# Performance work log

Hardware: AMD Instinct MI355X
Metric: run time of the kernel (lower is better)

## Reference

```python
import jax, jax.numpy as jnp
import numpy as np

B, N, M, K = 4, 8192, 2048, 8
F1, F2 = 256, 256


def _knn_idx(p1t, p2t, k):
    # p1t [B,N,3], p2t [B,M,3] -> idx [B,N,k] of k nearest points in p2t for each p1t point
    d = (jnp.sum(p1t ** 2, -1)[:, :, None]
         + jnp.sum(p2t ** 2, -1)[:, None, :]
         - 2.0 * jnp.einsum('bnc,bmc->bnm', p1t, p2t))
    _, idx = jax.lax.top_k(-d, k)
    return idx


def _gather(feat, idx):
    # feat [B,C,M], idx [B,N,K] -> [B,C,N,K]  (grouping_operation)
    return jax.vmap(lambda f, i: f[:, i])(feat, idx)


def setup_inputs() -> dict:
    key = jax.random.key(0)
    ks = jax.random.split(key, 16)
    rn = lambda k, s: jax.random.normal(k, s, dtype=jnp.float32)
    ru = lambda k, s: jax.random.uniform(k, s, dtype=jnp.float32)
    return {
        'pos1': rn(ks[0], (B, 3, N)),
        'pos2': rn(ks[1], (B, 3, M)),
        'feature1': rn(ks[2], (B, F1, N)),
        'feature2': rn(ks[3], (B, F2, M)),
        'w1_0': rn(ks[4], (128, F2 + 3)) * 0.05, 's1_0': ru(ks[5], (128,)), 'b1_0': rn(ks[6], (128,)) * 0.05,
        'w1_1': rn(ks[7], (128, 128)) * 0.05, 's1_1': ru(ks[8], (128,)), 'b1_1': rn(ks[9], (128,)) * 0.05,
        'w1_2': rn(ks[10], (256, 128)) * 0.05, 's1_2': ru(ks[11], (256,)), 'b1_2': rn(ks[12], (256,)) * 0.05,
        'w2_0': rn(ks[13], (256, 256 + F1)) * 0.05, 's2_0': ru(ks[14], (256,)), 'b2_0': rn(ks[15], (256,)) * 0.05,
    }


def reference(pos1, pos2, feature1, feature2,
              w1_0, s1_0, b1_0, w1_1, s1_1, b1_1, w1_2, s1_2, b1_2,
              w2_0, s2_0, b2_0):
    # KNN grouping (knn=True branch): neighbors of each pos1 point among pos2 points
    idx = _knn_idx(pos1.transpose(0, 2, 1), pos2.transpose(0, 2, 1), K)  # [B,N,K]
    pos2_grouped = _gather(pos2, idx)                 # [B,3,N,K]
    pos_diff = pos2_grouped - pos1[:, :, :, None]     # [B,3,N,K]
    feat2_grouped = _gather(feature2, idx)            # [B,F2,N,K]
    feat = jnp.concatenate([feat2_grouped, pos_diff], axis=1)  # [B,F2+3,N,K]
    # mlp1: 1x1 Conv2d (no bias) + BN(eval, folded scale/bias) + ReLU
    for w, s, b in ((w1_0, s1_0, b1_0), (w1_1, s1_1, b1_1), (w1_2, s1_2, b1_2)):
        feat = jax.nn.relu(jnp.einsum('oc,bcnk->bonk', w, feat)
                           * s[None, :, None, None] + b[None, :, None, None])
    feat = jnp.max(feat, axis=-1)                     # [B,256,N]
    feat = jnp.concatenate([feat, feature1], axis=1)  # [B,256+F1,N]
    # mlp2: 1x1 Conv1d (no bias) + BN + ReLU
    for w, s, b in ((w2_0, s2_0, b2_0),):
        feat = jax.nn.relu(jnp.einsum('oc,bcn->bon', w, feat)
                           * s[None, :, None] + b[None, :, None])
    return feat
```

## Files before the change

### kernel.cpp

```cpp
#include <hip/hip_runtime.h>
#include <hip/hip_bf16.h>

#define B_ 4
#define N_ 8192
#define M_ 2048
#define K_ 8

typedef __bf16 bf16x8 __attribute__((ext_vector_type(8)));
typedef __bf16 bf16x4 __attribute__((ext_vector_type(4)));
typedef float  floatx4 __attribute__((ext_vector_type(4)));
typedef unsigned long long u64k;

#define AS1G __attribute__((address_space(1)))
#define AS3L __attribute__((address_space(3)))

__device__ __forceinline__ void ce(u64k& a, u64k& b) {
  u64k lo = a < b ? a : b;
  u64k hi = a < b ? b : a;
  a = lo; b = hi;
}

__global__ __launch_bounds__(256) void pre_knn(
    const float* __restrict__ w10, const float* __restrict__ w11,
    const float* __restrict__ w12, const float* __restrict__ w20,
    const float* __restrict__ feature1, const float* __restrict__ feature2,
    const float* __restrict__ pos1, const float* __restrict__ pos2,
    __bf16* __restrict__ w0p, __bf16* __restrict__ w11b,
    __bf16* __restrict__ w12b, __bf16* __restrict__ w20b,
    __bf16* __restrict__ f2t, __bf16* __restrict__ f1t,
    u64k* __restrict__ part)
{
  __shared__ __align__(16) char smem[32768];
  const int bid = blockIdx.x;
  const int tid = threadIdx.x;

  if (bid < 1024) {
    floatx4* P = (floatx4*)smem;
    u64k (*md)[32] = (u64k(*)[32])(smem + 16384);
    const int b = (bid >> 7) & 3;
    const int half = bid >> 9;
    const int n0 = (bid & 127) * 64;
    const int cbase = half * 1024;

    const float* p2 = pos2 + b * 3 * M_;
    for (int i = tid; i < 1024; i += 256) {
      const int c = cbase + i;
      float x = p2[c], y = p2[M_ + c], z = p2[2 * M_ + c];
      floatx4 q;
      q[0] = x; q[1] = y; q[2] = z;
      q[3] = __fadd_rn(__fadd_rn(__fmul_rn(x, x), __fmul_rn(y, y)), __fmul_rn(z, z));
      P[i] = q;
    }
    __syncthreads();

    const int p = tid >> 2, t = tid & 3;
    const int n = n0 + p;
    const float* p1 = pos1 + b * 3 * N_;
    const float x1 = p1[n], y1 = p1[N_ + n], z1 = p1[2 * N_ + n];
    const float r1 = __fadd_rn(__fadd_rn(__fmul_rn(x1, x1), __fmul_rn(y1, y1)),
                               __fmul_rn(z1, z1));

    u64k bd[8];
    #pragma unroll
    for (int r = 0; r < 8; r++) bd[r] = ~0ULL;

    for (int bb = 0; bb < 32; ++bb) {
      floatx4 q[8];
      #pragma unroll
      for (int i = 0; i < 8; i++) q[i] = P[4 * (8 * bb + i) + t];

      u64k s[8];
      #pragma unroll
      for (int i = 0; i < 8; i++) {
        float dot = __fadd_rn(__fadd_rn(__fmul_rn(x1, q[i][0]), __fmul_rn(y1, q[i][1])),
                              __fmul_rn(z1, q[i][2]));
        float d = __fsub_rn(__fadd_rn(r1, q[i][3]), __fmul_rn(2.0f, dot));
        unsigned du = __float_as_uint(d);
        unsigned k32 = du ^ ((unsigned)((int)du >> 31) | 0x80000000u);
        s[i] = ((u64k)k32 << 11) | (unsigned)(cbase + 4 * (8 * bb + i) + t);
      }

      ce(s[0], s[1]); ce(s[2], s[3]); ce(s[4], s[5]); ce(s[6], s[7]);
      ce(s[0], s[2]); ce(s[1], s[3]); ce(s[4], s[6]); ce(s[5], s[7]);
      ce(s[1], s[2]); ce(s[5], s[6]);
      ce(s[0], s[4]); ce(s[1], s[5]); ce(s[2], s[6]); ce(s[3], s[7]);
      ce(s[2], s[4]); ce(s[3], s[5]);
      ce(s[1], s[2]); ce(s[3], s[4]); ce(s[5], s[6]);

      if (s[0] < bd[7]) {
        #pragma unroll
        for (int k = 0; k < 8; k++) { u64k x = s[7 - k]; bd[k] = bd[k] < x ? bd[k] : x; }
        ce(bd[0], bd[4]); ce(bd[1], bd[5]); ce(bd[2], bd[6]); ce(bd[3], bd[7]);
        ce(bd[0], bd[2]); ce(bd[1], bd[3]); ce(bd[4], bd[6]); ce(bd[5], bd[7]);
        ce(bd[0], bd[1]); ce(bd[2], bd[3]); ce(bd[4], bd[5]); ce(bd[6], bd[7]);
      }
    }

    {
      const int swp = (p & 3) << 3;
      #pragma unroll
      for (int r = 0; r < 8; r++) md[p][(t * 8 + r) ^ swp] = bd[r];
    }
    __syncthreads();

    if (tid < 64) {
      const int sw = tid & 3;
      const int b0 = (0 ^ sw) << 3, b1 = (1 ^ sw) << 3;
      const int b2 = (2 ^ sw) << 3, b3 = (3 ^ sw) << 3;
      int h0 = 0, h1 = 0, h2 = 0, h3 = 0;
      u64k* o = part + ((size_t)((b * 2 + half) * N_ + n0 + tid)) * 8;
      #pragma unroll
      for (int r = 0; r < 8; r++) {
        u64k k0 = md[tid][b0 + h0], k1 = md[tid][b1 + h1];
        u64k k2 = md[tid][b2 + h2], k3 = md[tid][b3 + h3];
        u64k m01 = k0 < k1 ? k0 : k1;
        u64k m23 = k2 < k3 ? k2 : k3;
        u64k m = m01 < m23 ? m01 : m23;
        h0 += (k0 == m); h1 += (k1 == m); h2 += (k2 == m); h3 += (k3 == m);
        o[r] = m;
      }
    }
  } else if (bid < 3072) {
    float (*tile)[33] = (float(*)[33])smem;
    const int tb = bid - 1024;
    const int C = 256, L = M_;
    const int b = tb >> 9;
    const int c0 = ((tb >> 6) & 7) * 32, l0 = (tb & 63) * 32;
    const int tx = tid & 31, ty = tid >> 5;
    const float* src = feature2 + (size_t)b * C * L;
    #pragma unroll
    for (int i = 0; i < 4; i++)
      tile[ty + 8 * i][tx] = src[(size_t)(c0 + ty + 8 * i) * L + l0 + tx];
    __syncthreads();
    __bf16* dst = f2t + (size_t)b * L * C;
    #pragma unroll
    for (int i = 0; i < 4; i++)
      dst[(size_t)(l0 + ty + 8 * i) * C + c0 + tx] = (__bf16)tile[tx][ty + 8 * i];
  } else if (bid < 11264) {
    float (*tile)[33] = (float(*)[33])smem;
    const int tb = bid - 3072;
    const int C = 256, L = N_;
    const int b = tb >> 11;
    const int c0 = ((tb >> 8) & 7) * 32, l0 = (tb & 255) * 32;
    const int tx = tid & 31, ty = tid >> 5;
    const float* src = feature1 + (size_t)b * C * L;
    #pragma unroll
    for (int i = 0; i < 4; i++)
      tile[ty + 8 * i][tx] = src[(size_t)(c0 + ty + 8 * i) * L + l0 + tx];
    __syncthreads();
    __bf16* dst = f1t + (size_t)b * L * C;
    #pragma unroll
    for (int i = 0; i < 4; i++)
      dst[(size_t)(l0 + ty + 8 * i) * C + c0 + tx] = (__bf16)tile[tx][ty + 8 * i];
  } else {
    int t = (bid - 11264) * 256 + tid;
    if (t < 36864) {
      int o = t / 288, c = t - o * 288;
      w0p[t] = (c < 259) ? (__bf16)w10[o * 259 + c] : (__bf16)0.0f;
    } else if (t < 53248) {
      int i = t - 36864; w11b[i] = (__bf16)w11[i];
    } else if (t < 86016) {
      int i = t - 53248; w12b[i] = (__bf16)w12[i];
    } else if (t < 217088) {
      int i = t - 86016; w20b[i] = (__bf16)w20[i];
    }
  }
}

__global__ __launch_bounds__(256) void knn_merge(
    const u64k* __restrict__ part, int* __restrict__ idx_out)
{
  const int pt = blockIdx.x * 256 + threadIdx.x;
  const int b = pt >> 13, n = pt & (N_ - 1);
  const u64k* a0 = part + ((size_t)((b * 2 + 0) * N_ + n)) * 8;
  const u64k* a1 = part + ((size_t)((b * 2 + 1) * N_ + n)) * 8;
  u64k av[8], cv[8];
  #pragma unroll
  for (int r = 0; r < 8; r++) { av[r] = a0[r]; cv[r] = a1[r]; }
  #pragma unroll
  for (int k = 0; k < 8; k++) { u64k x = cv[7 - k]; av[k] = av[k] < x ? av[k] : x; }
  ce(av[0], av[4]); ce(av[1], av[5]); ce(av[2], av[6]); ce(av[3], av[7]);
  ce(av[0], av[2]); ce(av[1], av[3]); ce(av[4], av[6]); ce(av[5], av[7]);
  ce(av[0], av[1]); ce(av[2], av[3]); ce(av[4], av[5]); ce(av[6], av[7]);
  int* o = idx_out + (size_t)pt * 8;
  #pragma unroll
  for (int r = 0; r < 8; r++) o[r] = (int)(av[r] & 2047u);
}

template <int KSTEPS>
__device__ __forceinline__ void mfma_kloop_swz(
    const __bf16* X, const __bf16* W, int wstride, int c0, int lane,
    floatx4 (&acc)[4][2])
{
  const int lrow = lane & 15, quad = lane >> 4;
  const floatx4 fz = {0.f, 0.f, 0.f, 0.f};
  #pragma unroll
  for (int pt = 0; pt < 4; pt++) { acc[pt][0] = fz; acc[pt][1] = fz; }

  bf16x8 wf0 = *(const bf16x8*)(W + (size_t)(c0 + lrow) * wstride + quad * 8);
  bf16x8 wf1 = *(const bf16x8*)(W + (size_t)(c0 + 16 + lrow) * wstride + quad * 8);
  bf16x8 xf[4];
  #pragma unroll
  for (int pt = 0; pt < 4; pt++) {
    const int row = pt * 16 + lrow;
    xf[pt] = *(const bf16x8*)((const char*)X + row * 256
                              + ((quad * 16) ^ ((row & 7) << 4)));
  }

  #pragma unroll
  for (int ks = 0; ks < KSTEPS; ks++) {
    bf16x8 wn0, wn1, xn[4];
    if (ks + 1 < KSTEPS) {
      const int kn = (ks + 1) * 32 + quad * 8;
      wn0 = *(const bf16x8*)(W + (size_t)(c0 + lrow) * wstride + kn);
      wn1 = *(const bf16x8*)(W + (size_t)(c0 + 16 + lrow) * wstride + kn);
      #pragma unroll
      for (int pt = 0; pt < 4; pt++) {
        const int row = pt * 16 + lrow;
        xn[pt] = *(const bf16x8*)((const char*)X + row * 256
                                  + (((ks + 1) * 64 + quad * 16) ^ ((row & 7) << 4)));
      }
    }
    #pragma unroll
    for (int pt = 0; pt < 4; pt++) {
      acc[pt][0] = __builtin_amdgcn_mfma_f32_16x16x32_bf16(wf0, xf[pt], acc[pt][0], 0, 0, 0);
      acc[pt][1] = __builtin_amdgcn_mfma_f32_16x16x32_bf16(wf1, xf[pt], acc[pt][1], 0, 0, 0);
    }
    if (ks + 1 < KSTEPS) {
      wf0 = wn0; wf1 = wn1;
      #pragma unroll
      for (int pt = 0; pt < 4; pt++) xf[pt] = xn[pt];
    }
  }
}

__global__ __launch_bounds__(256, 4) void mlp1_kernel(
    const float* __restrict__ pos1, const float* __restrict__ pos2,
    const int* __restrict__ idx, const __bf16* __restrict__ f2t,
    const __bf16* __restrict__ w0p, const float* __restrict__ s10, const float* __restrict__ b10,
    const __bf16* __restrict__ w11b, const float* __restrict__ s11, const float* __restrict__ b11,
    const __bf16* __restrict__ w12b, const float* __restrict__ s12, const float* __restrict__ b12,
    __bf16* __restrict__ maxed)
{
  __shared__ __align__(16) __bf16 Xs[64 * 256];
  __bf16* const Y1 = Xs;
  __bf16* const Y0 = Xs + 32 * 256;
  __bf16* const Mst = Xs + 32 * 256;

  const int b = blockIdx.y;
  const int n0 = blockIdx.x * 8;
  const int tid = threadIdx.x;
  const int wave = tid >> 6, lane = tid & 63;
  const int lrow = lane & 15, quad = lane >> 4;
  const int c0 = 32 * wave;
  const int idxbase = (b * N_ + n0) * K_;

  {
    const int r0 = wave * 16;
    const int hf = lane >> 5;
    const int ch = lane & 31;
    int mr[8];
    #pragma unroll
    for (int i = 0; i < 8; i++)
      mr[i] = idx[idxbase + r0 + 2 * i + hf];
    #pragma unroll
    for (int i = 0; i < 8; i++) {
      const int r = r0 + 2 * i + hf;
      const char* src = (const char*)f2t
          + (((size_t)(b * M_ + mr[i])) << 9)
          + ((ch << 4) ^ ((r & 7) << 4));
      __builtin_amdgcn_global_load_lds(
          (const AS1G unsigned int*)src,
          (AS3L unsigned int*)(Xs + (r0 + 2 * i) * 256),
          16, 0, 0);
    }
  }

  bf16x8 xlast[4];
  #pragma unroll
  for (int pt = 0; pt < 4; pt++) { bf16x8 v = {}; xlast[pt] = v; }
  if (quad == 0) {
    #pragma unroll
    for (int pt = 0; pt < 4; pt++) {
      const int r = pt * 16 + lrow;
      const int m = idx[idxbase + r];
      const int n = n0 + (r >> 3);
      bf16x8 v = {};
      v[0] = (__bf16)(pos2[b * 3 * M_ + m]          - pos1[b * 3 * N_ + n]);
      v[1] = (__bf16)(pos2[b * 3 * M_ + M_ + m]     - pos1[b * 3 * N_ + N_ + n]);
      v[2] = (__bf16)(pos2[b * 3 * M_ + 2 * M_ + m] - pos1[b * 3 * N_ + 2 * N_ + n]);
      xlast[pt] = v;
    }
  }

  bf16x8 wf0 = *(const bf16x8*)(w0p + (size_t)(c0 + lrow) * 288 + quad * 8);
  bf16x8 wf1 = *(const bf16x8*)(w0p + (size_t)(c0 + 16 + lrow) * 288 + quad * 8);

  __syncthreads();

  floatx4 acc[4][2];
  {
    const floatx4 fz = {0.f, 0.f, 0.f, 0.f};
    #pragma unroll
    for (int pt = 0; pt < 4; pt++) { acc[pt][0] = fz; acc[pt][1] = fz; }

    const int swz = (lrow & 7) << 4;
    bf16x8 xf[4];
    #pragma unroll
    for (int pt = 0; pt < 4; pt++)
      xf[pt] = *(const bf16x8*)((const char*)Xs + (pt * 16 + lrow) * 512
                                + ((quad * 16) ^ swz));

    #pragma unroll
    for (int ks = 0; ks < 9; ks++) {
      bf16x8 wn0, wn1, xn[4];
      if (ks < 8) {
        const int kn = (ks + 1) * 32 + quad * 8;
        wn0 = *(const bf16x8*)(w0p + (size_t)(c0 + lrow) * 288 + kn);
        wn1 = *(const bf16x8*)(w0p + (size_t)(c0 + 16 + lrow) * 288 + kn);
        if (ks < 7) {
          const int kb = ((ks + 1) * 64 + quad * 16) ^ swz;
          #pragma unroll
          for (int pt = 0; pt < 4; pt++)
            xn[pt] = *(const bf16x8*)((const char*)Xs + (pt * 16 + lrow) * 512 + kb);
        } else {
          #pragma unroll
          for (int pt = 0; pt < 4; pt++) xn[pt] = xlast[pt];
        }
      }
      #pragma unroll
      for (int pt = 0; pt < 4; pt++) {
        acc[pt][0] = __builtin_amdgcn_mfma_f32_16x16x32_bf16(wf0, xf[pt], acc[pt][0], 0, 0, 0);
        acc[pt][1] = __builtin_amdgcn_mfma_f32_16x16x32_bf16(wf1, xf[pt], acc[pt][1], 0, 0, 0);
      }
      if (ks < 8) {
        wf0 = wn0; wf1 = wn1;
        #pragma unroll
        for (int pt = 0; pt < 4; pt++) xf[pt] = xn[pt];
      }
    }
  }

  __syncthreads();

  #pragma unroll
  for (int pt = 0; pt < 4; pt++) {
    #pragma unroll
    for (int wt = 0; wt < 2; wt++) {
      const int colg = c0 + wt * 16 + quad * 4;
      floatx4 s4 = *(const floatx4*)(s10 + colg);
      floatx4 b4 = *(const floatx4*)(b10 + colg);
      bf16x4 pk;
      #pragma unroll
      for (int r = 0; r < 4; r++) {
        float v = acc[pt][wt][r] * s4[r] + b4[r];
        pk[r] = (__bf16)(v > 0.f ? v : 0.f);
      }
      const int row = pt * 16 + lrow;
      const int cb = colg * 2;
      *(bf16x4*)((char*)Y0 + row * 256
                 + ((cb & ~15) ^ ((row & 7) << 4)) + (cb & 15)) = pk;
    }
  }
  __syncthreads();

  {
    floatx4 a1c[4][2];
    mfma_kloop_swz<4>(Y0, w11b, 128, c0, lane, a1c);
    #pragma unroll
    for (int pt = 0; pt < 4; pt++) {
      #pragma unroll
      for (int wt = 0; wt < 2; wt++) {
        const int colg = c0 + wt * 16 + quad * 4;
        floatx4 s4 = *(const floatx4*)(s11 + colg);
        floatx4 b4 = *(const floatx4*)(b11 + colg);
        bf16x4 pk;
        #pragma unroll
        for (int r = 0; r < 4; r++) {
          float v = a1c[pt][wt][r] * s4[r] + b4[r];
          pk[r] = (__bf16)(v > 0.f ? v : 0.f);
        }
        const int row = pt * 16 + lrow;
        const int cb = colg * 2;
        *(bf16x4*)((char*)Y1 + row * 256
                   + ((cb & ~15) ^ ((row & 7) << 4)) + (cb & 15)) = pk;
      }
    }
  }
  __syncthreads();

  #pragma unroll
  for (int p = 0; p < 2; p++) {
    floatx4 a2c[4][2];
    mfma_kloop_swz<4>(Y1, w12b, 128, 128 * p + c0, lane, a2c);
    #pragma unroll
    for (int pt = 0; pt < 4; pt++) {
      #pragma unroll
      for (int wt = 0; wt < 2; wt++) {
        const int colg = 128 * p + c0 + wt * 16 + quad * 4;
        floatx4 s4 = *(const floatx4*)(s12 + colg);
        floatx4 b4 = *(const floatx4*)(b12 + colg);
        floatx4 v;
        #pragma unroll
        for (int r = 0; r < 4; r++) {
          float t = a2c[pt][wt][r] * s4[r] + b4[r];
          v[r] = t > 0.f ? t : 0.f;
        }
        #pragma unroll
        for (int st = 1; st <= 4; st <<= 1) {
          #pragma unroll
          for (int r = 0; r < 4; r++)
            v[r] = fmaxf(v[r], __shfl_xor(v[r], st, 64));
        }
        if ((lrow & 7) == 0) {
          const int point = pt * 2 + (lrow >> 3);
          bf16x4 pk;
          #pragma unroll
          for (int r = 0; r < 4; r++) pk[r] = (__bf16)v[r];
          *(bf16x4*)(Mst + point * 264 + colg) = pk;
        }
      }
    }
  }
  __syncthreads();

  {
    const int point = tid >> 5, ch = tid & 31;
    bf16x8 v = *(const bf16x8*)(Mst + point * 264 + ch * 8);
    *(bf16x8*)(maxed + ((size_t)(b * N_ + n0 + point)) * 256 + ch * 8) = v;
  }
}

__global__ __launch_bounds__(256, 3) void mlp2_kernel(
    const __bf16* __restrict__ maxed, const __bf16* __restrict__ f1t,
    const __bf16* __restrict__ w20b, const float* __restrict__ s20,
    const float* __restrict__ b20, float* __restrict__ out)
{
  __shared__ __align__(16) __bf16 As[2][32 * 256];
  const int rows0 = blockIdx.x * 32;
  const int b = rows0 >> 13;
  const int nbase = rows0 & (N_ - 1);
  const int tid = threadIdx.x;
  const int wave = tid >> 6, lane = tid & 63;
  const int lrow = lane & 15, quad = lane >> 4;
  const int c0 = 64 * wave;

  {
    const int r0 = wave * 8;
    const int hf = lane >> 5, ch = lane & 31;
    #pragma unroll
    for (int i = 0; i < 4; i++) {
      const int r = r0 + 2 * i + hf;
      const size_t srow = ((size_t)(rows0 + r)) << 9;
      const int so = (ch << 4) ^ ((r & 7) << 4);
      __builtin_amdgcn_global_load_lds(
          (const AS1G unsigned int*)((const char*)maxed + srow + so),
          (AS3L unsigned int*)(&As[0][(r0 + 2 * i) * 256]), 16, 0, 0);
      __builtin_amdgcn_global_load_lds(
          (const AS1G unsigned int*)((const char*)f1t + srow + so),
          (AS3L unsigned int*)(&As[1][(r0 + 2 * i) * 256]), 16, 0, 0);
    }
  }

  bf16x8 wf[4];
  #pragma unroll
  for (int wt = 0; wt < 4; wt++)
    wf[wt] = *(const bf16x8*)(w20b + (size_t)(c0 + wt * 16 + lrow) * 512 + quad * 8);

  __syncthreads();

  floatx4 acc[2][4];
  const floatx4 fz = {0.f, 0.f, 0.f, 0.f};
  #pragma unroll
  for (int mt = 0; mt < 2; mt++)
    #pragma unroll
    for (int wt = 0; wt < 4; wt++) acc[mt][wt] = fz;

  auto aaddr = [&](int ks, int mt) -> const char* {
    const int row = mt * 16 + lrow;
    return (const char*)(&As[ks >> 3][0]) + row * 512
           + ((((ks & 7) * 64) + quad * 16) ^ ((row & 7) << 4));
  };

  bf16x8 af[2];
  af[0] = *(const bf16x8*)aaddr(0, 0);
  af[1] = *(const bf16x8*)aaddr(0, 1);

  #pragma unroll
  for (int ks = 0; ks < 16; ks++) {
    bf16x8 wn[4], an[2];
    if (ks < 15) {
      const int kn = (ks + 1) * 32 + quad * 8;
      #pragma unroll
      for (int wt = 0; wt < 4; wt++)
        wn[wt] = *(const bf16x8*)(w20b + (size_t)(c0 + wt * 16 + lrow) * 512 + kn);
      an[0] = *(const bf16x8*)aaddr(ks + 1, 0);
      an[1] = *(const bf16x8*)aaddr(ks + 1, 1);
    }
    #pragma unroll
    for (int mt = 0; mt < 2; mt++)
      #pragma unroll
      for (int wt = 0; wt < 4; wt++)
        acc[mt][wt] = __builtin_amdgcn_mfma_f32_16x16x32_bf16(af[mt], wf[wt], acc[mt][wt], 0, 0, 0);
    if (ks < 15) {
      #pragma unroll
      for (int wt = 0; wt < 4; wt++) wf[wt] = wn[wt];
      af[0] = an[0]; af[1] = an[1];
    }
  }

  #pragma unroll
  for (int wt = 0; wt < 4; wt++) {
    const int col = c0 + wt * 16 + lrow;
    const float s = s20[col];
    const float bb = b20[col];
    #pragma unroll
    for (int mt = 0; mt < 2; mt++) {
      floatx4 pk;
      #pragma unroll
      for (int r = 0; r < 4; r++) {
        float v = acc[mt][wt][r] * s + bb;
        pk[r] = v > 0.f ? v : 0.f;
      }
      const int n = nbase + mt * 16 + quad * 4;
      *(floatx4*)(out + ((size_t)(b * 256 + col)) * N_ + n) = pk;
    }
  }
}

extern "C" void kernel_launch(void* const* d_in, const int* in_sizes, int n_in,
                              void* d_out, int out_size, void* d_ws, size_t ws_size,
                              hipStream_t stream)
{
  const float* pos1     = (const float*)d_in[0];
  const float* pos2     = (const float*)d_in[1];
  const float* feature1 = (const float*)d_in[2];
  const float* feature2 = (const float*)d_in[3];
  const float* w1_0 = (const float*)d_in[4];
  const float* s1_0 = (const float*)d_in[5];
  const float* b1_0 = (const float*)d_in[6];
  const float* w1_1 = (const float*)d_in[7];
  const float* s1_1 = (const float*)d_in[8];
  const float* b1_1 = (const float*)d_in[9];
  const float* w1_2 = (const float*)d_in[10];
  const float* s1_2 = (const float*)d_in[11];
  const float* b1_2 = (const float*)d_in[12];
  const float* w2_0 = (const float*)d_in[13];
  const float* s2_0 = (const float*)d_in[14];
  const float* b2_0 = (const float*)d_in[15];

  char* ws = (char*)d_ws;
  int*    idx   = (int*)(ws);
  __bf16* f2t   = (__bf16*)(ws + 1048576);
  __bf16* f1t   = (__bf16*)(ws + 5242880);
  __bf16* maxed = (__bf16*)(ws + 22020096);
  __bf16* w0p   = (__bf16*)(ws + 38797312);
  __bf16* w11b  = (__bf16*)(ws + 38871040);
  __bf16* w12b  = (__bf16*)(ws + 38903808);
  __bf16* w20b  = (__bf16*)(ws + 38969344);
  u64k*   part  = (u64k*)(ws + 22020096);

  pre_knn<<<dim3(12112), 256, 0, stream>>>(
      w1_0, w1_1, w1_2, w2_0, feature1, feature2, pos1, pos2,
      w0p, w11b, w12b, w20b, f2t, f1t, part);
  knn_merge<<<dim3(N_ * B_ / 256), 256, 0, stream>>>(part, idx);
  mlp1_kernel<<<dim3(N_ / 8, B_), 256, 0, stream>>>(
      pos1, pos2, idx, f2t, w0p, s1_0, b1_0, w11b, s1_1, b1_1, w12b, s1_2, b1_2, maxed);
  mlp2_kernel<<<dim3(N_ * B_ / 32), 256, 0, stream>>>(maxed, f1t, w20b, s2_0, b2_0,
                                                      (float*)d_out);
}
```

Measured before the change: 306.0 us.

## Split KNN candidate search into quarters and merge four partial top-8 lists

The KNN pre-pass now splits each batch's 2048 candidate points into four 512-point chunks instead of two. That doubles the number of search blocks and halves the serial loop length per block, which should improve load balance and occupancy. The merge kernel now reads four partial sorted lists per query and combines them with a tree of bitonic merges, adding partial-buffer traffic and merge work. The mlp1 kernel's launch-bounds occupancy hint is also lowered from 4 to 3, which gives it more registers per thread.

```diff
diff --git a/kernel.cpp b/kernel.cpp
--- a/kernel.cpp
+++ b/kernel.cpp
@@ -18,6 +18,14 @@
   u64k lo = a < b ? a : b;
   u64k hi = a < b ? b : a;
   a = lo; b = hi;
+}
+
+__device__ __forceinline__ void merge8(u64k (&a)[8], const u64k (&c)[8]) {
+  #pragma unroll
+  for (int k = 0; k < 8; k++) { u64k x = c[7 - k]; a[k] = a[k] < x ? a[k] : x; }
+  ce(a[0], a[4]); ce(a[1], a[5]); ce(a[2], a[6]); ce(a[3], a[7]);
+  ce(a[0], a[2]); ce(a[1], a[3]); ce(a[4], a[6]); ce(a[5], a[7]);
+  ce(a[0], a[1]); ce(a[2], a[3]); ce(a[4], a[5]); ce(a[6], a[7]);
 }
 
 __global__ __launch_bounds__(256) void pre_knn(
@@ -30,20 +38,20 @@
     __bf16* __restrict__ f2t, __bf16* __restrict__ f1t,
     u64k* __restrict__ part)
 {
-  __shared__ __align__(16) char smem[32768];
+  __shared__ __align__(16) char smem[24576];
   const int bid = blockIdx.x;
   const int tid = threadIdx.x;
 
-  if (bid < 1024) {
+  if (bid < 2048) {
     floatx4* P = (floatx4*)smem;
-    u64k (*md)[32] = (u64k(*)[32])(smem + 16384);
+    u64k (*md)[32] = (u64k(*)[32])(smem + 8192);
     const int b = (bid >> 7) & 3;
-    const int half = bid >> 9;
+    const int quarter = bid >> 9;
     const int n0 = (bid & 127) * 64;
-    const int cbase = half * 1024;
+    const int cbase = quarter * 512;
 
     const float* p2 = pos2 + b * 3 * M_;
-    for (int i = tid; i < 1024; i += 256) {
+    for (int i = tid; i < 512; i += 256) {
       const int c = cbase + i;
       float x = p2[c], y = p2[M_ + c], z = p2[2 * M_ + c];
       floatx4 q;
@@ -64,7 +72,7 @@
     #pragma unroll
     for (int r = 0; r < 8; r++) bd[r] = ~0ULL;
 
-    for (int bb = 0; bb < 32; ++bb) {
+    for (int bb = 0; bb < 16; ++bb) {
       floatx4 q[8];
       #pragma unroll
       for (int i = 0; i < 8; i++) q[i] = P[4 * (8 * bb + i) + t];
@@ -87,13 +95,7 @@
       ce(s[2], s[4]); ce(s[3], s[5]);
       ce(s[1], s[2]); ce(s[3], s[4]); ce(s[5], s[6]);
 
-      if (s[0] < bd[7]) {
-        #pragma unroll
-        for (int k = 0; k < 8; k++) { u64k x = s[7 - k]; bd[k] = bd[k] < x ? bd[k] : x; }
-        ce(bd[0], bd[4]); ce(bd[1], bd[5]); ce(bd[2], bd[6]); ce(bd[3], bd[7]);
-        ce(bd[0], bd[2]); ce(bd[1], bd[3]); ce(bd[4], bd[6]); ce(bd[5], bd[7]);
-        ce(bd[0], bd[1]); ce(bd[2], bd[3]); ce(bd[4], bd[5]); ce(bd[6], bd[7]);
-      }
+      if (s[0] < bd[7]) merge8(bd, s);
     }
 
     {
@@ -108,7 +110,7 @@
       const int b0 = (0 ^ sw) << 3, b1 = (1 ^ sw) << 3;
       const int b2 = (2 ^ sw) << 3, b3 = (3 ^ sw) << 3;
       int h0 = 0, h1 = 0, h2 = 0, h3 = 0;
-      u64k* o = part + ((size_t)((b * 2 + half) * N_ + n0 + tid)) * 8;
+      u64k* o = part + ((size_t)((b * 4 + quarter) * N_ + n0 + tid)) * 8;
       #pragma unroll
       for (int r = 0; r < 8; r++) {
         u64k k0 = md[tid][b0 + h0], k1 = md[tid][b1 + h1];
@@ -120,9 +122,9 @@
         o[r] = m;
       }
     }
-  } else if (bid < 3072) {
+  } else if (bid < 4096) {
     float (*tile)[33] = (float(*)[33])smem;
-    const int tb = bid - 1024;
+    const int tb = bid - 2048;
     const int C = 256, L = M_;
     const int b = tb >> 9;
     const int c0 = ((tb >> 6) & 7) * 32, l0 = (tb & 63) * 32;
@@ -136,9 +138,9 @@
     #pragma unroll
     for (int i = 0; i < 4; i++)
       dst[(size_t)(l0 + ty + 8 * i) * C + c0 + tx] = (__bf16)tile[tx][ty + 8 * i];
-  } else if (bid < 11264) {
+  } else if (bid < 12288) {
     float (*tile)[33] = (float(*)[33])smem;
-    const int tb = bid - 3072;
+    const int tb = bid - 4096;
     const int C = 256, L = N_;
     const int b = tb >> 11;
     const int c0 = ((tb >> 8) & 7) * 32, l0 = (tb & 255) * 32;
@@ -153,7 +155,7 @@
     for (int i = 0; i < 4; i++)
       dst[(size_t)(l0 + ty + 8 * i) * C + c0 + tx] = (__bf16)tile[tx][ty + 8 * i];
   } else {
-    int t = (bid - 11264) * 256 + tid;
+    int t = (bid - 12288) * 256 + tid;
     if (t < 36864) {
       int o = t / 288, c = t - o * 288;
       w0p[t] = (c < 259) ? (__bf16)w10[o * 259 + c] : (__bf16)0.0f;
@@ -172,19 +174,23 @@
 {
   const int pt = blockIdx.x * 256 + threadIdx.x;
   const int b = pt >> 13, n = pt & (N_ - 1);
-  const u64k* a0 = part + ((size_t)((b * 2 + 0) * N_ + n)) * 8;
-  const u64k* a1 = part + ((size_t)((b * 2 + 1) * N_ + n)) * 8;
-  u64k av[8], cv[8];
-  #pragma unroll
-  for (int r = 0; r < 8; r++) { av[r] = a0[r]; cv[r] = a1[r]; }
-  #pragma unroll
-  for (int k = 0; k < 8; k++) { u64k x = cv[7 - k]; av[k] = av[k] < x ? av[k] : x; }
-  ce(av[0], av[4]); ce(av[1], av[5]); ce(av[2], av[6]); ce(av[3], av[7]);
-  ce(av[0], av[2]); ce(av[1], av[3]); ce(av[4], av[6]); ce(av[5], av[7]);
-  ce(av[0], av[1]); ce(av[2], av[3]); ce(av[4], av[5]); ce(av[6], av[7]);
+  u64k a01[8], c1[8], a23[8], c3[8];
+  {
+    const u64k* l0 = part + ((size_t)((b * 4 + 0) * N_ + n)) * 8;
+    const u64k* l1 = part + ((size_t)((b * 4 + 1) * N_ + n)) * 8;
+    const u64k* l2 = part + ((size_t)((b * 4 + 2) * N_ + n)) * 8;
+    const u64k* l3 = part + ((size_t)((b * 4 + 3) * N_ + n)) * 8;
+    #pragma unroll
+    for (int r = 0; r < 8; r++) {
+      a01[r] = l0[r]; c1[r] = l1[r]; a23[r] = l2[r]; c3[r] = l3[r];
+    }
+  }
+  merge8(a01, c1);
+  merge8(a23, c3);
+  merge8(a01, a23);
   int* o = idx_out + (size_t)pt * 8;
   #pragma unroll
-  for (int r = 0; r < 8; r++) o[r] = (int)(av[r] & 2047u);
+  for (int r = 0; r < 8; r++) o[r] = (int)(a01[r] & 2047u);
 }
 
 template <int KSTEPS>
@@ -234,7 +240,7 @@
   }
 }
 
-__global__ __launch_bounds__(256, 4) void mlp1_kernel(
+__global__ __launch_bounds__(256, 3) void mlp1_kernel(
     const float* __restrict__ pos1, const float* __restrict__ pos2,
     const int* __restrict__ idx, const __bf16* __restrict__ f2t,
     const __bf16* __restrict__ w0p, const float* __restrict__ s10, const float* __restrict__ b10,
@@ -560,7 +566,7 @@
   __bf16* w20b  = (__bf16*)(ws + 38969344);
   u64k*   part  = (u64k*)(ws + 22020096);
 
-  pre_knn<<<dim3(12112), 256, 0, stream>>>(
+  pre_knn<<<dim3(13136), 256, 0, stream>>>(
       w1_0, w1_1, w1_2, w2_0, feature1, feature2, pos1, pos2,
       w0p, w11b, w12b, w20b, f2t, f1t, part);
   knn_merge<<<dim3(N_ * B_ / 256), 256, 0, stream>>>(part, idx);
```

Result: no change. 308.9 us (+0.9%).
